# Optimization experiments

Measured on AMD Instinct MI355X. Metric: run time of the kernel, lower is better.

## Reference

```python
import jax, jax.numpy as jnp
import numpy as np

WS = 8        # window_size
SHIFT = 4     # shift_size
HEADS = 3
DIM = 96
EPS = 1e-5

# static relative coordinates for one window (matches torch.meshgrid default 'ij')
_coords = np.stack(np.meshgrid(np.arange(WS), np.arange(WS), indexing='ij'))  # [2,ws,ws]
_flat = _coords.reshape(2, -1)                                               # [2,N]
_rel = _flat[:, :, None] - _flat[:, None, :]                                  # [2,N,N]
REL_ABS_SUM = jnp.asarray(np.abs(_rel[0]) + np.abs(_rel[1]), dtype=np.float32)  # [N,N]


def _layernorm(x, g, b):
    m = jnp.mean(x, axis=-1, keepdims=True)
    v = jnp.mean((x - m) ** 2, axis=-1, keepdims=True)
    return (x - m) * jax.lax.rsqrt(v + EPS) * g + b


def _band_shift(x, s):
    # x: [B,C,H,W]. Each band of WS rows: even band index -> roll +s along W, odd -> roll -s.
    B, C, H, W = x.shape
    xb = x.reshape(B, C, H // WS, WS, W)
    ev = jnp.roll(xb, s, axis=-1)
    od = jnp.roll(xb, -s, axis=-1)
    parity = (jnp.arange(H // WS) % 2 == 1).reshape(1, 1, -1, 1, 1)
    return jnp.where(parity, od, ev).reshape(B, C, H, W)


def _window_partition(x):
    # [B,C,H,W] -> [B*nH*nW, WS*WS, C]
    B, C, H, W = x.shape
    x = x.reshape(B, C, H // WS, WS, W // WS, WS)
    x = x.transpose(0, 2, 4, 3, 5, 1)
    return x.reshape(-1, WS * WS, C)


def _window_reverse(w, B, H, W, C):
    # [B*nH*nW, WS*WS, C] -> [B,C,H,W]
    x = w.reshape(B, H // WS, W // WS, WS, WS, C)
    x = x.transpose(0, 5, 1, 3, 2, 4)
    return x.reshape(B, C, H, W)


def setup_inputs() -> dict:
    key = jax.random.key(0)
    ks = jax.random.split(key, 8)
    d = DIM
    return {
        'x': jax.random.normal(ks[0], (2, d, 512, 512), jnp.float32),
        'ln1_g': jnp.ones((d,), jnp.float32),
        'ln1_b': jnp.zeros((d,), jnp.float32),
        'qkv_w': jax.random.normal(ks[1], (3 * d, d), jnp.float32) * 0.02,
        'qkv_b': jnp.zeros((3 * d,), jnp.float32),
        'lap_A': jnp.float32(1.0),
        'lap_B': jnp.float32(1.0),
        'proj_w': jax.random.normal(ks[2], (d, d), jnp.float32) * 0.02,
        'proj_b': jnp.zeros((d,), jnp.float32),
        'ln2_g': jnp.ones((d,), jnp.float32),
        'ln2_b': jnp.zeros((d,), jnp.float32),
        'mlp_w1': jax.random.normal(ks[3], (4 * d, d), jnp.float32) * 0.02,
        'mlp_b1': jnp.zeros((4 * d,), jnp.float32),
        'mlp_w2': jax.random.normal(ks[4], (d, 4 * d), jnp.float32) * 0.02,
        'mlp_b2': jnp.zeros((d,), jnp.float32),
    }


def reference(x, ln1_g, ln1_b, qkv_w, qkv_b, lap_A, lap_B, proj_w, proj_b,
              ln2_g, ln2_b, mlp_w1, mlp_b1, mlp_w2, mlp_b2):
    B, C, H, W = x.shape
    hd = C // HEADS
    scale = hd ** -0.5

    tokens = x.transpose(0, 2, 3, 1).reshape(B, H * W, C)  # [B,HW,C]
    shortcut = tokens
    xn = _layernorm(tokens, ln1_g, ln1_b)
    xn = xn.reshape(B, H, W, C).transpose(0, 3, 1, 2)       # [B,C,H,W]

    xs = _band_shift(xn, SHIFT)
    win = _window_partition(xs)                             # [Bw, N, C]

    # window attention
    Bw, N, _ = win.shape
    qkv = win @ qkv_w.T + qkv_b                             # [Bw,N,3C]
    qkv = qkv.reshape(Bw, N, 3, HEADS, hd)
    q = qkv[:, :, 0].transpose(0, 2, 1, 3) * scale          # [Bw,h,N,hd]
    k = qkv[:, :, 1].transpose(0, 2, 1, 3)
    v = qkv[:, :, 2].transpose(0, 2, 1, 3)
    attn = jnp.einsum('bhnd,bhmd->bhnm', q, k)              # [Bw,h,N,N]
    bias = (lap_A ** 2) * jnp.exp(-0.5 * (REL_ABS_SUM / (lap_B ** 2)))  # [N,N]
    attn = jax.nn.softmax(attn + bias[None, None], axis=-1)
    out = jnp.einsum('bhnm,bhmd->bhnd', attn, v)            # [Bw,h,N,hd]
    out = out.transpose(0, 2, 1, 3).reshape(Bw, N, C)
    out = out @ proj_w.T + proj_b

    xr = _window_reverse(out, B, H, W, C)                   # [B,C,H,W]
    xr = _band_shift(xr, -SHIFT)                            # inverse shift

    xt = xr.transpose(0, 2, 3, 1).reshape(B, H * W, C)
    xt = shortcut + xt
    h1 = _layernorm(xt, ln2_g, ln2_b)
    h1 = jax.nn.gelu(h1 @ mlp_w1.T + mlp_b1, approximate=False)
    xt = xt + (h1 @ mlp_w2.T + mlp_b2)

    return xt.reshape(B, H, W, C).transpose(0, 3, 1, 2)
```

## Files before the change

kernel.cpp:

```cpp
#include <hip/hip_runtime.h>

#define SHIFT 4

typedef short bf16x8 __attribute__((ext_vector_type(8)));
typedef float f32x4  __attribute__((ext_vector_type(4)));

#define MFMA(a, b, c) __builtin_amdgcn_mfma_f32_16x16x32_bf16((a), (b), (c), 0, 0, 0)

__device__ __forceinline__ unsigned short f2bf(float f) {
  unsigned int u = __float_as_uint(f);
  u += 0x7fffu + ((u >> 16) & 1u);
  return (unsigned short)(u >> 16);
}
__device__ __forceinline__ float bf2f(unsigned short u) {
  return __uint_as_float(((unsigned int)u) << 16);
}

__global__ void k_cvt(const float* __restrict__ s, unsigned short* __restrict__ d, int n) {
  int i = blockIdx.x * blockDim.x + threadIdx.x;
  int st = gridDim.x * blockDim.x;
  for (; i < n; i += st) d[i] = f2bf(s[i]);
}

__global__ void k_cvt_p1(const float* __restrict__ s, unsigned short* __restrict__ d) {
  int i = blockIdx.x * 256 + threadIdx.x;
  if (i < 36864) {
    int col = i / 96, k = i - col * 96;
    d[(((col >> 4) * 3 + (k >> 5)) << 9) + ((col & 15) << 5) + (k & 31)] = f2bf(s[i]);
  }
}
__global__ void k_cvt_p2(const float* __restrict__ s, unsigned short* __restrict__ d) {
  int i = blockIdx.x * 256 + threadIdx.x;
  if (i < 36864) {
    int col = i / 384, k = i - col * 384;
    d[(((col >> 4) * 12 + (k >> 5)) << 9) + ((col & 15) << 5) + (k & 31)] = f2bf(s[i]);
  }
}

__global__ __launch_bounds__(256, 8) void k_pre(
    const float* __restrict__ x, unsigned short* __restrict__ X)
{
  __shared__ __align__(16) unsigned short xls[64 * 104];
  const int tid = threadIdx.x;
  const int bid = blockIdx.x;
  const int b  = bid >> 12;
  const int h  = (bid >> 3) & 511;
  const int w0 = (bid & 7) << 6;

#pragma unroll
  for (int v = 0; v < 6; ++v) {
    int idx4 = v * 256 + tid;
    int c    = idx4 >> 4;
    int p4   = (idx4 & 15) << 2;
    const float4 f = *reinterpret_cast<const float4*>(
        &x[((size_t)(b * 96 + c) << 18) + (h << 9) + w0 + p4]);
    xls[(p4 + 0) * 104 + c] = f2bf(f.x);
    xls[(p4 + 1) * 104 + c] = f2bf(f.y);
    xls[(p4 + 2) * 104 + c] = f2bf(f.z);
    xls[(p4 + 3) * 104 + c] = f2bf(f.w);
  }
  __syncthreads();
  const int q = tid & 3, t = tid >> 2;
  unsigned short* Xo = &X[(size_t)((b << 18) + (h << 9) + w0 + t) * 96 + q * 24];
#pragma unroll
  for (int v = 0; v < 3; ++v)
    *reinterpret_cast<bf16x8*>(&Xo[v * 8]) =
        *reinterpret_cast<const bf16x8*>(&xls[t * 104 + q * 24 + v * 8]);
}

__global__ __launch_bounds__(256, 4) void k_attn(
    const float* __restrict__ ln1g, const float* __restrict__ ln1b,
    const unsigned short* __restrict__ qkvw,
    const float* __restrict__ qkvb,
    const float* __restrict__ lapA, const float* __restrict__ lapB,
    const unsigned short* __restrict__ projw,
    const float* __restrict__ projb,
    unsigned short* __restrict__ X)
{
  __shared__ __align__(16) unsigned short R1[64 * 104];
  __shared__ __align__(16) unsigned short Ks[64 * 104];
  __shared__ __align__(16) unsigned short Vt[96 * 72];

  const int tid = threadIdx.x;
  const int wid = blockIdx.x;
  const int b   = wid >> 12;
  const int hi  = (wid >> 6) & 63;
  const int wi  = wid & 63;
  const int q   = tid & 3;
  const int t   = tid >> 2;
  const int lane = tid & 63;
  const int wv   = tid >> 6;
  const int l16  = lane & 15;
  const int lg   = lane >> 4;
  const int arow = wv * 16 + l16;
  const f32x4 zz = {0.f, 0.f, 0.f, 0.f};

  const int sh = ((hi & 1) == 0) ? -SHIFT : SHIFT;

  const int ftok = wv * 16 + l16;
  const int fhh = hi * 8 + (ftok >> 3);
  const int fww = ((wi * 8 + (ftok & 7)) + sh) & 511;
  const unsigned short* xfp = &X[(size_t)((b << 18) + (fhh << 9) + fww) * 96 + lg * 8];

  float xv[24];
#pragma unroll
  for (int ks = 0; ks < 3; ++ks) {
    bf16x8 g = *reinterpret_cast<const bf16x8*>(&xfp[ks * 32]);
#pragma unroll
    for (int e = 0; e < 8; ++e) xv[ks * 8 + e] = bf2f((unsigned short)g[e]);
  }
  float mu, rs;
  {
    float s1 = 0.f, s2 = 0.f;
#pragma unroll
    for (int k = 0; k < 24; ++k) { float v = xv[k]; s1 += v; s2 += v * v; }
    s1 += __shfl_xor(s1, 16); s2 += __shfl_xor(s2, 16);
    s1 += __shfl_xor(s1, 32); s2 += __shfl_xor(s2, 32);
    mu = s1 * (1.f / 96.f);
    rs = rsqrtf(s2 * (1.f / 96.f) - mu * mu + 1e-5f);
  }
  bf16x8 afr[3];
#pragma unroll
  for (int ks = 0; ks < 3; ++ks) {
#pragma unroll
    for (int e = 0; e < 8; ++e) {
      int c = ks * 32 + lg * 8 + e;
      afr[ks][e] = (short)f2bf((xv[ks * 8 + e] - mu) * rs * ln1g[c] + ln1b[c]);
    }
  }

  const float qscale = 0.17677669529663687f;
#pragma unroll
  for (int nt = 0; nt < 6; ++nt) {
    int col = nt * 16 + l16;
    f32x4 acc = zz;
#pragma unroll
    for (int ks = 0; ks < 3; ++ks)
      acc = MFMA(afr[ks], *reinterpret_cast<const bf16x8*>(&qkvw[col * 96 + ks * 32 + lg * 8]), acc);
    float bc = qkvb[col];
#pragma unroll
    for (int j = 0; j < 4; ++j)
      R1[(wv * 16 + lg * 4 + j) * 104 + col] = f2bf((acc[j] + bc) * qscale);
  }
#pragma unroll
  for (int nt = 0; nt < 6; ++nt) {
    int col = 96 + nt * 16 + l16;
    f32x4 acc = zz;
#pragma unroll
    for (int ks = 0; ks < 3; ++ks)
      acc = MFMA(afr[ks], *reinterpret_cast<const bf16x8*>(&qkvw[col * 96 + ks * 32 + lg * 8]), acc);
    float bc = qkvb[col];
#pragma unroll
    for (int j = 0; j < 4; ++j)
      Ks[(wv * 16 + lg * 4 + j) * 104 + nt * 16 + l16] = f2bf(acc[j] + bc);
  }
#pragma unroll
  for (int nt = 0; nt < 6; ++nt) {
    int col = 192 + nt * 16 + l16;
    f32x4 acc = zz;
#pragma unroll
    for (int ks = 0; ks < 3; ++ks)
      acc = MFMA(afr[ks], *reinterpret_cast<const bf16x8*>(&qkvw[col * 96 + ks * 32 + lg * 8]), acc);
    float bc = qkvb[col];
#pragma unroll
    for (int j = 0; j < 4; ++j)
      Vt[(nt * 16 + l16) * 72 + wv * 16 + lg * 4 + j] = f2bf(acc[j] + bc);
  }
  __syncthreads();

  float bias_r[4][4];
  {
    const float a = lapA[0], bb = lapB[0];
    const float A2 = a * a;
    const float nh = -0.5f / (bb * bb);
#pragma unroll
    for (int j = 0; j < 4; ++j) {
      int qi = wv * 16 + lg * 4 + j;
      int qr = qi >> 3, qc = qi & 7;
#pragma unroll
      for (int kt = 0; kt < 4; ++kt) {
        int key = kt * 16 + l16;
        int dd = abs(qr - (key >> 3)) + abs(qc - (key & 7));
        bias_r[j][kt] = A2 * __expf(nh * (float)dd);
      }
    }
  }

  bf16x8 aqh[3];
#pragma unroll
  for (int h = 0; h < 3; ++h)
    aqh[h] = *reinterpret_cast<const bf16x8*>(&R1[arow * 104 + h * 32 + lg * 8]);

  f32x4 oacc[6];
#pragma unroll
  for (int i = 0; i < 6; ++i) oacc[i] = zz;

#pragma unroll 1
  for (int h = 0; h < 3; ++h) {
    f32x4 sc[4];
#pragma unroll
    for (int kt = 0; kt < 4; ++kt) {
      bf16x8 bk = *reinterpret_cast<const bf16x8*>(&Ks[(kt * 16 + l16) * 104 + h * 32 + lg * 8]);
      sc[kt] = MFMA(aqh[h], bk, zz);
    }
#pragma unroll
    for (int j = 0; j < 4; ++j) {
      int qi = wv * 16 + lg * 4 + j;
      float e0 = __expf(sc[0][j] + bias_r[j][0]);
      float e1 = __expf(sc[1][j] + bias_r[j][1]);
      float e2 = __expf(sc[2][j] + bias_r[j][2]);
      float e3 = __expf(sc[3][j] + bias_r[j][3]);
      float s = e0 + e1 + e2 + e3;
#pragma unroll
      for (int off = 1; off < 16; off <<= 1) s += __shfl_xor(s, off);
      float inv = 1.0f / s;
      R1[qi * 104 +  0 + l16] = f2bf(e0 * inv);
      R1[qi * 104 + 16 + l16] = f2bf(e1 * inv);
      R1[qi * 104 + 32 + l16] = f2bf(e2 * inv);
      R1[qi * 104 + 48 + l16] = f2bf(e3 * inv);
    }
    bf16x8 ap0 = *reinterpret_cast<const bf16x8*>(&R1[arow * 104 +  0 + lg * 8]);
    bf16x8 ap1 = *reinterpret_cast<const bf16x8*>(&R1[arow * 104 + 32 + lg * 8]);
#pragma unroll
    for (int dt = 0; dt < 2; ++dt) {
      int vcol = h * 32 + dt * 16 + l16;
      bf16x8 bv0 = *reinterpret_cast<const bf16x8*>(&Vt[vcol * 72 +  0 + lg * 8]);
      bf16x8 bv1 = *reinterpret_cast<const bf16x8*>(&Vt[vcol * 72 + 32 + lg * 8]);
      oacc[h * 2 + dt] = MFMA(ap0, bv0, oacc[h * 2 + dt]);
      oacc[h * 2 + dt] = MFMA(ap1, bv1, oacc[h * 2 + dt]);
    }
  }
#pragma unroll
  for (int i = 0; i < 6; ++i)
#pragma unroll
    for (int j = 0; j < 4; ++j)
      R1[(wv * 16 + lg * 4 + j) * 104 + i * 16 + l16] = f2bf(oacc[i][j]);

  bf16x8 ao[3];
#pragma unroll
  for (int ks = 0; ks < 3; ++ks)
    ao[ks] = *reinterpret_cast<const bf16x8*>(&R1[arow * 104 + ks * 32 + lg * 8]);
#pragma unroll
  for (int nt = 0; nt < 6; ++nt) {
    int col = nt * 16 + l16;
    f32x4 acc = zz;
#pragma unroll
    for (int ks = 0; ks < 3; ++ks)
      acc = MFMA(ao[ks], *reinterpret_cast<const bf16x8*>(&projw[col * 96 + ks * 32 + lg * 8]), acc);
    float pb = projb[col];
#pragma unroll
    for (int j = 0; j < 4; ++j)
      R1[(wv * 16 + lg * 4 + j) * 104 + col] = f2bf(acc[j] + pb);
  }
  {
    const int hh2 = hi * 8 + (t >> 3);
    const int ww2 = ((wi * 8 + (t & 7)) + sh) & 511;
    unsigned short* xg = &X[(size_t)((b << 18) + (hh2 << 9) + ww2) * 96 + q * 24];
#pragma unroll
    for (int v = 0; v < 3; ++v) {
      bf16x8 m  = *reinterpret_cast<const bf16x8*>(&R1[t * 104 + q * 24 + v * 8]);
      bf16x8 xr = *reinterpret_cast<const bf16x8*>(&xg[v * 8]);
      bf16x8 pk;
#pragma unroll
      for (int e = 0; e < 8; ++e)
        pk[e] = (short)f2bf(bf2f((unsigned short)m[e]) + bf2f((unsigned short)xr[e]));
      *reinterpret_cast<bf16x8*>(&xg[v * 8]) = pk;
    }
  }
}

__global__ __launch_bounds__(512, 2) void k_mlp(
    const unsigned short* __restrict__ X,
    const float* __restrict__ ln2g, const float* __restrict__ ln2b,
    const unsigned short* __restrict__ w1p,
    const float* __restrict__ b1,
    const unsigned short* __restrict__ w2p,
    const float* __restrict__ b2,
    float* __restrict__ out)
{
  __shared__ __align__(16) unsigned short Wl[36864];
  __shared__ __align__(16) unsigned short W2l[34816];
  __shared__ __align__(16) unsigned short Hl[128 * 72];

  const int tid = threadIdx.x;
  const int q    = tid & 3;
  const int t    = tid >> 2;
  const int lane = tid & 63;
  const int wv   = tid >> 6;
  const int l16  = lane & 15;
  const int lg   = lane >> 4;
  const f32x4 zz = {0.f, 0.f, 0.f, 0.f};

#pragma unroll
  for (int it = 0; it < 9; ++it) {
    int v8 = it * 512 + tid;
    *reinterpret_cast<bf16x8*>(&Wl[v8 * 8]) = *reinterpret_cast<const bf16x8*>(&w1p[v8 * 8]);
    if (v8 < 4352)
      *reinterpret_cast<bf16x8*>(&W2l[v8 * 8]) = *reinterpret_cast<const bf16x8*>(&w2p[v8 * 8]);
  }
  bf16x8 wfr[4];
#pragma unroll
  for (int r = 0; r < 4; ++r)
    wfr[r] = *reinterpret_cast<const bf16x8*>(&w2p[((68 + r) << 9) + (l16 << 5) + lg * 8]);

  float gr[24], br[24], b1r[24], b2r[6];
#pragma unroll
  for (int i = 0; i < 24; ++i) {
    int c = (i >> 3) * 32 + lg * 8 + (i & 7);
    gr[i] = ln2g[c]; br[i] = ln2b[c];
  }
#pragma unroll
  for (int i = 0; i < 24; ++i) b1r[i] = b1[i * 16 + l16];
#pragma unroll
  for (int i = 0; i < 6; ++i) b2r[i] = b2[i * 16 + l16];

  __syncthreads();

#pragma unroll 1
  for (int s = 0; s < 8; ++s) {
    const int stb = (blockIdx.x * 8 + s) * 128;

    const unsigned short* xfp = &X[(size_t)(stb + wv * 16 + l16) * 96 + lg * 8];
    float xv[24];
#pragma unroll
    for (int ks = 0; ks < 3; ++ks) {
      bf16x8 g = *reinterpret_cast<const bf16x8*>(&xfp[ks * 32]);
#pragma unroll
      for (int e = 0; e < 8; ++e) xv[ks * 8 + e] = bf2f((unsigned short)g[e]);
    }
    float mu, rs;
    {
      float s1 = 0.f, s2 = 0.f;
#pragma unroll
      for (int k = 0; k < 24; ++k) { float v = xv[k]; s1 += v; s2 += v * v; }
      s1 += __shfl_xor(s1, 16); s2 += __shfl_xor(s2, 16);
      s1 += __shfl_xor(s1, 32); s2 += __shfl_xor(s2, 32);
      mu = s1 * (1.f / 96.f);
      rs = rsqrtf(s2 * (1.f / 96.f) - mu * mu + 1e-5f);
    }
    bf16x8 a1[3];
#pragma unroll
    for (int ks = 0; ks < 3; ++ks)
#pragma unroll
      for (int e = 0; e < 8; ++e)
        a1[ks][e] = (short)f2bf((xv[ks * 8 + e] - mu) * rs * gr[ks * 8 + e] + br[ks * 8 + e]);

    f32x4 acc2[6];
#pragma unroll
    for (int i = 0; i < 6; ++i) acc2[i] = zz;

#pragma unroll
    for (int ch = 0; ch < 6; ++ch) {
#pragma unroll
      for (int nt = 0; nt < 4; ++nt) {
        const int ntg = ch * 4 + nt;
        f32x4 acc = zz;
#pragma unroll
        for (int ks = 0; ks < 3; ++ks)
          acc = MFMA(a1[ks],
                     *reinterpret_cast<const bf16x8*>(&Wl[((ntg * 3 + ks) << 9) + (l16 << 5) + lg * 8]),
                     acc);
        float bb = b1r[ntg];
#pragma unroll
        for (int j = 0; j < 4; ++j) {
          float v = acc[j] + bb;
          float tt = v * fmaf(0.071354816f, v * v, 1.5957691f);
          float g = v * __builtin_amdgcn_rcpf(1.f + __expf(-tt));
          Hl[(wv * 16 + lg * 4 + j) * 72 + nt * 16 + l16] = f2bf(g);
        }
      }
      bf16x8 ah0 = *reinterpret_cast<const bf16x8*>(&Hl[(wv * 16 + l16) * 72 + lg * 8]);
      bf16x8 ah1 = *reinterpret_cast<const bf16x8*>(&Hl[(wv * 16 + l16) * 72 + 32 + lg * 8]);
#pragma unroll
      for (int nt = 0; nt < 6; ++nt) {
        const int t0 = nt * 12 + ch * 2;
        const int t1 = t0 + 1;
        bf16x8 bf0 = (t0 >= 68) ? wfr[(t0 - 68) & 3]
                   : *reinterpret_cast<const bf16x8*>(&W2l[(t0 << 9) + (l16 << 5) + lg * 8]);
        bf16x8 bf1 = (t1 >= 68) ? wfr[(t1 - 68) & 3]
                   : *reinterpret_cast<const bf16x8*>(&W2l[(t1 << 9) + (l16 << 5) + lg * 8]);
        acc2[nt] = MFMA(ah0, bf0, acc2[nt]);
        acc2[nt] = MFMA(ah1, bf1, acc2[nt]);
      }
    }

    const int tok = stb + t;
    const unsigned short* xrp = &X[(size_t)tok * 96 + q * 24];
    const int bb_ = tok >> 18;
    const int pix = tok & 262143;
#pragma unroll
    for (int pass = 0; pass < 2; ++pass) {
#pragma unroll
      for (int ntl = 0; ntl < 3; ++ntl) {
        const int nt = pass * 3 + ntl;
#pragma unroll
        for (int j = 0; j < 4; ++j)
          Hl[(wv * 16 + lg * 4 + j) * 72 + ntl * 16 + l16] = f2bf(acc2[nt][j] + b2r[nt]);
      }
      if ((q >> 1) == pass) {
        const int lc = (q & 1) * 24;
#pragma unroll
        for (int v = 0; v < 3; ++v) {
          bf16x8 m  = *reinterpret_cast<const bf16x8*>(&Hl[t * 72 + lc + v * 8]);
          bf16x8 xr = *reinterpret_cast<const bf16x8*>(&xrp[v * 8]);
#pragma unroll
          for (int e = 0; e < 8; ++e) {
            int c = q * 24 + v * 8 + e;
            out[((size_t)(bb_ * 96 + c) << 18) + pix] =
                bf2f((unsigned short)m[e]) + bf2f((unsigned short)xr[e]);
          }
        }
      }
    }
  }
}

extern "C" void kernel_launch(void* const* d_in, const int* in_sizes, int n_in,
                              void* d_out, int out_size, void* d_ws, size_t ws_size,
                              hipStream_t stream) {
  const float* x     = (const float*)d_in[0];
  const float* ln1g  = (const float*)d_in[1];
  const float* ln1b  = (const float*)d_in[2];
  const float* qkv_w = (const float*)d_in[3];
  const float* qkv_b = (const float*)d_in[4];
  const float* lapA  = (const float*)d_in[5];
  const float* lapB  = (const float*)d_in[6];
  const float* prj_w = (const float*)d_in[7];
  const float* prj_b = (const float*)d_in[8];
  const float* ln2g  = (const float*)d_in[9];
  const float* ln2b  = (const float*)d_in[10];
  const float* w1f   = (const float*)d_in[11];
  const float* b1    = (const float*)d_in[12];
  const float* w2f   = (const float*)d_in[13];
  const float* b2    = (const float*)d_in[14];

  char* ws = (char*)d_ws;
  unsigned short* X     = (unsigned short*)ws;
  unsigned short* qkvwb = (unsigned short*)(ws + 100663296);
  unsigned short* prjwb = (unsigned short*)(ws + 100718592);
  unsigned short* w1p   = (unsigned short*)(ws + 100737024);
  unsigned short* w2p   = (unsigned short*)(ws + 100810752);

  k_cvt   <<<64, 256, 0, stream>>>(qkv_w, qkvwb, 288 * 96);
  k_cvt   <<<64, 256, 0, stream>>>(prj_w, prjwb, 96 * 96);
  k_cvt_p1<<<144, 256, 0, stream>>>(w1f, w1p);
  k_cvt_p2<<<144, 256, 0, stream>>>(w2f, w2p);

  k_pre <<<8192, 256, 0, stream>>>(x, X);
  k_attn<<<8192, 256, 0, stream>>>(ln1g, ln1b, qkvwb, qkv_b, lapA, lapB,
                                   prjwb, prj_b, X);
  k_mlp <<<512, 512, 0, stream>>>(X, ln2g, ln2b, w1p, b1, w2p, b2,
                                  (float*)d_out);
}
```

Measured before the change: 512.6 us.

## Batch weight loads, reuse register residual, move barrier after bias compute

The QKV and projection GEMMs now load weight fragments in batches of nine before issuing MFMAs, so global load latency overlaps instead of serialising per tile. The residual add reuses the x values already held in registers from the LayerNorm load and writes back through the same per-lane pointer, which removes a second global read of X. The barrier moves after the bias computation, and f2bf now uses the HIP intrinsic conversion. Holding nine weight fragments raises register pressure, and each lane now writes R1 rows it did not produce itself, which relies on the barriers that already exist.

```diff
diff --git a/kernel.cpp b/kernel.cpp
--- a/kernel.cpp
+++ b/kernel.cpp
@@ -1,4 +1,5 @@
 #include <hip/hip_runtime.h>
+#include <hip/hip_bf16.h>
 
 #define SHIFT 4
 
@@ -8,9 +9,8 @@
 #define MFMA(a, b, c) __builtin_amdgcn_mfma_f32_16x16x32_bf16((a), (b), (c), 0, 0, 0)
 
 __device__ __forceinline__ unsigned short f2bf(float f) {
-  unsigned int u = __float_as_uint(f);
-  u += 0x7fffu + ((u >> 16) & 1u);
-  return (unsigned short)(u >> 16);
+  __hip_bfloat16 h = __float2bfloat16(f);
+  return __hip_bfloat16_raw(h).x;
 }
 __device__ __forceinline__ float bf2f(unsigned short u) {
   return __uint_as_float(((unsigned int)u) << 16);
@@ -86,8 +86,6 @@
   const int b   = wid >> 12;
   const int hi  = (wid >> 6) & 63;
   const int wi  = wid & 63;
-  const int q   = tid & 3;
-  const int t   = tid >> 2;
   const int lane = tid & 63;
   const int wv   = tid >> 6;
   const int l16  = lane & 15;
@@ -100,7 +98,7 @@
   const int ftok = wv * 16 + l16;
   const int fhh = hi * 8 + (ftok >> 3);
   const int fww = ((wi * 8 + (ftok & 7)) + sh) & 511;
-  const unsigned short* xfp = &X[(size_t)((b << 18) + (fhh << 9) + fww) * 96 + lg * 8];
+  unsigned short* xfp = &X[(size_t)((b << 18) + (fhh << 9) + fww) * 96 + lg * 8];
 
   float xv[24];
 #pragma unroll
@@ -131,42 +129,67 @@
 
   const float qscale = 0.17677669529663687f;
 #pragma unroll
-  for (int nt = 0; nt < 6; ++nt) {
-    int col = nt * 16 + l16;
-    f32x4 acc = zz;
-#pragma unroll
-    for (int ks = 0; ks < 3; ++ks)
-      acc = MFMA(afr[ks], *reinterpret_cast<const bf16x8*>(&qkvw[col * 96 + ks * 32 + lg * 8]), acc);
-    float bc = qkvb[col];
-#pragma unroll
-    for (int j = 0; j < 4; ++j)
-      R1[(wv * 16 + lg * 4 + j) * 104 + col] = f2bf((acc[j] + bc) * qscale);
-  }
-#pragma unroll
-  for (int nt = 0; nt < 6; ++nt) {
-    int col = 96 + nt * 16 + l16;
-    f32x4 acc = zz;
-#pragma unroll
-    for (int ks = 0; ks < 3; ++ks)
-      acc = MFMA(afr[ks], *reinterpret_cast<const bf16x8*>(&qkvw[col * 96 + ks * 32 + lg * 8]), acc);
-    float bc = qkvb[col];
-#pragma unroll
-    for (int j = 0; j < 4; ++j)
-      Ks[(wv * 16 + lg * 4 + j) * 104 + nt * 16 + l16] = f2bf(acc[j] + bc);
-  }
-#pragma unroll
-  for (int nt = 0; nt < 6; ++nt) {
-    int col = 192 + nt * 16 + l16;
-    f32x4 acc = zz;
-#pragma unroll
-    for (int ks = 0; ks < 3; ++ks)
-      acc = MFMA(afr[ks], *reinterpret_cast<const bf16x8*>(&qkvw[col * 96 + ks * 32 + lg * 8]), acc);
-    float bc = qkvb[col];
-#pragma unroll
-    for (int j = 0; j < 4; ++j)
-      Vt[(nt * 16 + l16) * 72 + wv * 16 + lg * 4 + j] = f2bf(acc[j] + bc);
-  }
-  __syncthreads();
+  for (int half = 0; half < 2; ++half) {
+    bf16x8 wf[9];
+#pragma unroll
+    for (int i = 0; i < 9; ++i) {
+      int col = (half * 3 + i / 3) * 16 + l16;
+      wf[i] = *reinterpret_cast<const bf16x8*>(&qkvw[col * 96 + (i % 3) * 32 + lg * 8]);
+    }
+#pragma unroll
+    for (int ntl = 0; ntl < 3; ++ntl) {
+      int col = (half * 3 + ntl) * 16 + l16;
+      f32x4 acc = zz;
+#pragma unroll
+      for (int ks = 0; ks < 3; ++ks) acc = MFMA(afr[ks], wf[ntl * 3 + ks], acc);
+      float bc = qkvb[col];
+#pragma unroll
+      for (int j = 0; j < 4; ++j)
+        R1[(wv * 16 + lg * 4 + j) * 104 + col] = f2bf((acc[j] + bc) * qscale);
+    }
+  }
+#pragma unroll
+  for (int half = 0; half < 2; ++half) {
+    bf16x8 wf[9];
+#pragma unroll
+    for (int i = 0; i < 9; ++i) {
+      int col = 96 + (half * 3 + i / 3) * 16 + l16;
+      wf[i] = *reinterpret_cast<const bf16x8*>(&qkvw[col * 96 + (i % 3) * 32 + lg * 8]);
+    }
+#pragma unroll
+    for (int ntl = 0; ntl < 3; ++ntl) {
+      int nt = half * 3 + ntl;
+      int col = 96 + nt * 16 + l16;
+      f32x4 acc = zz;
+#pragma unroll
+      for (int ks = 0; ks < 3; ++ks) acc = MFMA(afr[ks], wf[ntl * 3 + ks], acc);
+      float bc = qkvb[col];
+#pragma unroll
+      for (int j = 0; j < 4; ++j)
+        Ks[(wv * 16 + lg * 4 + j) * 104 + nt * 16 + l16] = f2bf(acc[j] + bc);
+    }
+  }
+#pragma unroll
+  for (int half = 0; half < 2; ++half) {
+    bf16x8 wf[9];
+#pragma unroll
+    for (int i = 0; i < 9; ++i) {
+      int col = 192 + (half * 3 + i / 3) * 16 + l16;
+      wf[i] = *reinterpret_cast<const bf16x8*>(&qkvw[col * 96 + (i % 3) * 32 + lg * 8]);
+    }
+#pragma unroll
+    for (int ntl = 0; ntl < 3; ++ntl) {
+      int nt = half * 3 + ntl;
+      int col = 192 + nt * 16 + l16;
+      f32x4 acc = zz;
+#pragma unroll
+      for (int ks = 0; ks < 3; ++ks) acc = MFMA(afr[ks], wf[ntl * 3 + ks], acc);
+      float bc = qkvb[col];
+#pragma unroll
+      for (int j = 0; j < 4; ++j)
+        Vt[(nt * 16 + l16) * 72 + wv * 16 + lg * 4 + j] = f2bf(acc[j] + bc);
+    }
+  }
 
   float bias_r[4][4];
   {
@@ -185,6 +208,7 @@
       }
     }
   }
+  __syncthreads();
 
   bf16x8 aqh[3];
 #pragma unroll
@@ -241,31 +265,33 @@
   for (int ks = 0; ks < 3; ++ks)
     ao[ks] = *reinterpret_cast<const bf16x8*>(&R1[arow * 104 + ks * 32 + lg * 8]);
 #pragma unroll
-  for (int nt = 0; nt < 6; ++nt) {
-    int col = nt * 16 + l16;
-    f32x4 acc = zz;
-#pragma unroll
-    for (int ks = 0; ks < 3; ++ks)
-      acc = MFMA(ao[ks], *reinterpret_cast<const bf16x8*>(&projw[col * 96 + ks * 32 + lg * 8]), acc);
-    float pb = projb[col];
-#pragma unroll
-    for (int j = 0; j < 4; ++j)
-      R1[(wv * 16 + lg * 4 + j) * 104 + col] = f2bf(acc[j] + pb);
-  }
-  {
-    const int hh2 = hi * 8 + (t >> 3);
-    const int ww2 = ((wi * 8 + (t & 7)) + sh) & 511;
-    unsigned short* xg = &X[(size_t)((b << 18) + (hh2 << 9) + ww2) * 96 + q * 24];
-#pragma unroll
-    for (int v = 0; v < 3; ++v) {
-      bf16x8 m  = *reinterpret_cast<const bf16x8*>(&R1[t * 104 + q * 24 + v * 8]);
-      bf16x8 xr = *reinterpret_cast<const bf16x8*>(&xg[v * 8]);
-      bf16x8 pk;
-#pragma unroll
-      for (int e = 0; e < 8; ++e)
-        pk[e] = (short)f2bf(bf2f((unsigned short)m[e]) + bf2f((unsigned short)xr[e]));
-      *reinterpret_cast<bf16x8*>(&xg[v * 8]) = pk;
-    }
+  for (int half = 0; half < 2; ++half) {
+    bf16x8 wf[9];
+#pragma unroll
+    for (int i = 0; i < 9; ++i) {
+      int col = (half * 3 + i / 3) * 16 + l16;
+      wf[i] = *reinterpret_cast<const bf16x8*>(&projw[col * 96 + (i % 3) * 32 + lg * 8]);
+    }
+#pragma unroll
+    for (int ntl = 0; ntl < 3; ++ntl) {
+      int col = (half * 3 + ntl) * 16 + l16;
+      f32x4 acc = zz;
+#pragma unroll
+      for (int ks = 0; ks < 3; ++ks) acc = MFMA(ao[ks], wf[ntl * 3 + ks], acc);
+      float pb = projb[col];
+#pragma unroll
+      for (int j = 0; j < 4; ++j)
+        R1[(wv * 16 + lg * 4 + j) * 104 + col] = f2bf(acc[j] + pb);
+    }
+  }
+#pragma unroll
+  for (int ks = 0; ks < 3; ++ks) {
+    bf16x8 m = *reinterpret_cast<const bf16x8*>(&R1[ftok * 104 + ks * 32 + lg * 8]);
+    bf16x8 pk;
+#pragma unroll
+    for (int e = 0; e < 8; ++e)
+      pk[e] = (short)f2bf(bf2f((unsigned short)m[e]) + xv[ks * 8 + e]);
+    *reinterpret_cast<bf16x8*>(&xfp[ks * 32]) = pk;
   }
 }
 
```

Result: no change. 513.4 us (+0.2%).

## Make attention kernel persistent with LDS-resident packed weights and prefetch

Applied to the files above, without the earlier changes.

The attention kernel becomes persistent: 256 blocks of 512 threads, each holding two window groups that loop over 16 windows. The QKV and projection weights are repacked into an MFMA-friendly tiled layout and loaded into LDS once per block instead of being read from global memory per window. LayerNorm parameters and biases are hoisted into registers, and the next window's input is prefetched during attention. The residual now reuses the input values already held in registers instead of re-reading X. The cost is one block per CU with heavy LDS use, extra barriers, and possibly lower latency hiding.

```diff
diff --git a/kernel.cpp b/kernel.cpp
--- a/kernel.cpp
+++ b/kernel.cpp
@@ -1,4 +1,5 @@
 #include <hip/hip_runtime.h>
+#include <hip/hip_bf16.h>
 
 #define SHIFT 4
 
@@ -8,23 +9,16 @@
 #define MFMA(a, b, c) __builtin_amdgcn_mfma_f32_16x16x32_bf16((a), (b), (c), 0, 0, 0)
 
 __device__ __forceinline__ unsigned short f2bf(float f) {
-  unsigned int u = __float_as_uint(f);
-  u += 0x7fffu + ((u >> 16) & 1u);
-  return (unsigned short)(u >> 16);
+  __hip_bfloat16 h = __float2bfloat16(f);
+  return __hip_bfloat16_raw(h).x;
 }
 __device__ __forceinline__ float bf2f(unsigned short u) {
   return __uint_as_float(((unsigned int)u) << 16);
 }
 
-__global__ void k_cvt(const float* __restrict__ s, unsigned short* __restrict__ d, int n) {
-  int i = blockIdx.x * blockDim.x + threadIdx.x;
-  int st = gridDim.x * blockDim.x;
-  for (; i < n; i += st) d[i] = f2bf(s[i]);
-}
-
-__global__ void k_cvt_p1(const float* __restrict__ s, unsigned short* __restrict__ d) {
+__global__ void k_cvt_pt(const float* __restrict__ s, unsigned short* __restrict__ d, int n) {
   int i = blockIdx.x * 256 + threadIdx.x;
-  if (i < 36864) {
+  if (i < n) {
     int col = i / 96, k = i - col * 96;
     d[(((col >> 4) * 3 + (k >> 5)) << 9) + ((col & 15) << 5) + (k & 31)] = f2bf(s[i]);
   }
@@ -68,105 +62,62 @@
         *reinterpret_cast<const bf16x8*>(&xls[t * 104 + q * 24 + v * 8]);
 }
 
-__global__ __launch_bounds__(256, 4) void k_attn(
+__global__ __launch_bounds__(512, 1) void k_attn(
     const float* __restrict__ ln1g, const float* __restrict__ ln1b,
-    const unsigned short* __restrict__ qkvw,
+    const unsigned short* __restrict__ qkvwp,
     const float* __restrict__ qkvb,
     const float* __restrict__ lapA, const float* __restrict__ lapB,
-    const unsigned short* __restrict__ projw,
+    const unsigned short* __restrict__ projwp,
     const float* __restrict__ projb,
     unsigned short* __restrict__ X)
 {
-  __shared__ __align__(16) unsigned short R1[64 * 104];
-  __shared__ __align__(16) unsigned short Ks[64 * 104];
-  __shared__ __align__(16) unsigned short Vt[96 * 72];
-
-  const int tid = threadIdx.x;
-  const int wid = blockIdx.x;
-  const int b   = wid >> 12;
-  const int hi  = (wid >> 6) & 63;
-  const int wi  = wid & 63;
-  const int q   = tid & 3;
-  const int t   = tid >> 2;
+  __shared__ __align__(16) unsigned short WqkvL[27648];
+  __shared__ __align__(16) unsigned short WprojL[9216];
+  __shared__ __align__(16) unsigned short R1s[2][6656];
+  __shared__ __align__(16) unsigned short Kss[2][6656];
+  __shared__ __align__(16) unsigned short Vts[2][6912];
+
+  const int tid  = threadIdx.x;
   const int lane = tid & 63;
-  const int wv   = tid >> 6;
+  const int wv8  = tid >> 6;
+  const int g    = wv8 >> 2;
+  const int wvg  = wv8 & 3;
   const int l16  = lane & 15;
   const int lg   = lane >> 4;
-  const int arow = wv * 16 + l16;
+  const int arow = wvg * 16 + l16;
   const f32x4 zz = {0.f, 0.f, 0.f, 0.f};
 
-  const int sh = ((hi & 1) == 0) ? -SHIFT : SHIFT;
-
-  const int ftok = wv * 16 + l16;
-  const int fhh = hi * 8 + (ftok >> 3);
-  const int fww = ((wi * 8 + (ftok & 7)) + sh) & 511;
-  const unsigned short* xfp = &X[(size_t)((b << 18) + (fhh << 9) + fww) * 96 + lg * 8];
-
-  float xv[24];
-#pragma unroll
-  for (int ks = 0; ks < 3; ++ks) {
-    bf16x8 g = *reinterpret_cast<const bf16x8*>(&xfp[ks * 32]);
-#pragma unroll
-    for (int e = 0; e < 8; ++e) xv[ks * 8 + e] = bf2f((unsigned short)g[e]);
-  }
-  float mu, rs;
-  {
-    float s1 = 0.f, s2 = 0.f;
-#pragma unroll
-    for (int k = 0; k < 24; ++k) { float v = xv[k]; s1 += v; s2 += v * v; }
-    s1 += __shfl_xor(s1, 16); s2 += __shfl_xor(s2, 16);
-    s1 += __shfl_xor(s1, 32); s2 += __shfl_xor(s2, 32);
-    mu = s1 * (1.f / 96.f);
-    rs = rsqrtf(s2 * (1.f / 96.f) - mu * mu + 1e-5f);
-  }
-  bf16x8 afr[3];
-#pragma unroll
-  for (int ks = 0; ks < 3; ++ks) {
-#pragma unroll
-    for (int e = 0; e < 8; ++e) {
-      int c = ks * 32 + lg * 8 + e;
-      afr[ks][e] = (short)f2bf((xv[ks * 8 + e] - mu) * rs * ln1g[c] + ln1b[c]);
-    }
-  }
-
-  const float qscale = 0.17677669529663687f;
-#pragma unroll
-  for (int nt = 0; nt < 6; ++nt) {
-    int col = nt * 16 + l16;
-    f32x4 acc = zz;
-#pragma unroll
-    for (int ks = 0; ks < 3; ++ks)
-      acc = MFMA(afr[ks], *reinterpret_cast<const bf16x8*>(&qkvw[col * 96 + ks * 32 + lg * 8]), acc);
-    float bc = qkvb[col];
-#pragma unroll
-    for (int j = 0; j < 4; ++j)
-      R1[(wv * 16 + lg * 4 + j) * 104 + col] = f2bf((acc[j] + bc) * qscale);
-  }
-#pragma unroll
-  for (int nt = 0; nt < 6; ++nt) {
-    int col = 96 + nt * 16 + l16;
-    f32x4 acc = zz;
-#pragma unroll
-    for (int ks = 0; ks < 3; ++ks)
-      acc = MFMA(afr[ks], *reinterpret_cast<const bf16x8*>(&qkvw[col * 96 + ks * 32 + lg * 8]), acc);
-    float bc = qkvb[col];
-#pragma unroll
-    for (int j = 0; j < 4; ++j)
-      Ks[(wv * 16 + lg * 4 + j) * 104 + nt * 16 + l16] = f2bf(acc[j] + bc);
-  }
-#pragma unroll
-  for (int nt = 0; nt < 6; ++nt) {
-    int col = 192 + nt * 16 + l16;
-    f32x4 acc = zz;
-#pragma unroll
-    for (int ks = 0; ks < 3; ++ks)
-      acc = MFMA(afr[ks], *reinterpret_cast<const bf16x8*>(&qkvw[col * 96 + ks * 32 + lg * 8]), acc);
-    float bc = qkvb[col];
-#pragma unroll
-    for (int j = 0; j < 4; ++j)
-      Vt[(nt * 16 + l16) * 72 + wv * 16 + lg * 4 + j] = f2bf(acc[j] + bc);
-  }
-  __syncthreads();
+  unsigned short* R1 = R1s[g];
+  unsigned short* Ks = Kss[g];
+  unsigned short* Vt = Vts[g];
+
+#pragma unroll
+  for (int it = 0; it < 7; ++it) {
+    int v8 = it * 512 + tid;
+    if (v8 < 3456)
+      *reinterpret_cast<bf16x8*>(&WqkvL[v8 * 8]) =
+          *reinterpret_cast<const bf16x8*>(&qkvwp[v8 * 8]);
+  }
+#pragma unroll
+  for (int it = 0; it < 3; ++it) {
+    int v8 = it * 512 + tid;
+    if (v8 < 1152)
+      *reinterpret_cast<bf16x8*>(&WprojL[v8 * 8]) =
+          *reinterpret_cast<const bf16x8*>(&projwp[v8 * 8]);
+  }
+
+  float gl[24], bl[24];
+#pragma unroll
+  for (int i = 0; i < 24; ++i) {
+    int c = (i >> 3) * 32 + lg * 8 + (i & 7);
+    gl[i] = ln1g[c]; bl[i] = ln1b[c];
+  }
+  float qb[18];
+#pragma unroll
+  for (int nt = 0; nt < 18; ++nt) qb[nt] = qkvb[nt * 16 + l16];
+  float pbr[6];
+#pragma unroll
+  for (int nt = 0; nt < 6; ++nt) pbr[nt] = projb[nt * 16 + l16];
 
   float bias_r[4][4];
   {
@@ -175,7 +126,7 @@
     const float nh = -0.5f / (bb * bb);
 #pragma unroll
     for (int j = 0; j < 4; ++j) {
-      int qi = wv * 16 + lg * 4 + j;
+      int qi = wvg * 16 + lg * 4 + j;
       int qr = qi >> 3, qc = qi & 7;
 #pragma unroll
       for (int kt = 0; kt < 4; ++kt) {
@@ -185,87 +136,165 @@
       }
     }
   }
-
-  bf16x8 aqh[3];
-#pragma unroll
-  for (int h = 0; h < 3; ++h)
-    aqh[h] = *reinterpret_cast<const bf16x8*>(&R1[arow * 104 + h * 32 + lg * 8]);
-
-  f32x4 oacc[6];
-#pragma unroll
-  for (int i = 0; i < 6; ++i) oacc[i] = zz;
+  __syncthreads();
+
+  const float qscale = 0.17677669529663687f;
+  const int ftok = wvg * 16 + l16;
+
+  auto xaddr = [&](int w) -> unsigned short* {
+    int b  = w >> 12;
+    int hi = (w >> 6) & 63;
+    int wi = w & 63;
+    int sh = ((hi & 1) == 0) ? -SHIFT : SHIFT;
+    int fhh = hi * 8 + (ftok >> 3);
+    int fww = ((wi * 8 + (ftok & 7)) + sh) & 511;
+    return &X[(size_t)((b << 18) + (fhh << 9) + fww) * 96 + lg * 8];
+  };
+
+  int w = blockIdx.x * 32 + g;
+  unsigned short* xfp = xaddr(w);
+  bf16x8 xn[3];
+#pragma unroll
+  for (int ks = 0; ks < 3; ++ks)
+    xn[ks] = *reinterpret_cast<const bf16x8*>(&xfp[ks * 32]);
 
 #pragma unroll 1
-  for (int h = 0; h < 3; ++h) {
-    f32x4 sc[4];
-#pragma unroll
-    for (int kt = 0; kt < 4; ++kt) {
-      bf16x8 bk = *reinterpret_cast<const bf16x8*>(&Ks[(kt * 16 + l16) * 104 + h * 32 + lg * 8]);
-      sc[kt] = MFMA(aqh[h], bk, zz);
-    }
-#pragma unroll
-    for (int j = 0; j < 4; ++j) {
-      int qi = wv * 16 + lg * 4 + j;
-      float e0 = __expf(sc[0][j] + bias_r[j][0]);
-      float e1 = __expf(sc[1][j] + bias_r[j][1]);
-      float e2 = __expf(sc[2][j] + bias_r[j][2]);
-      float e3 = __expf(sc[3][j] + bias_r[j][3]);
-      float s = e0 + e1 + e2 + e3;
-#pragma unroll
-      for (int off = 1; off < 16; off <<= 1) s += __shfl_xor(s, off);
-      float inv = 1.0f / s;
-      R1[qi * 104 +  0 + l16] = f2bf(e0 * inv);
-      R1[qi * 104 + 16 + l16] = f2bf(e1 * inv);
-      R1[qi * 104 + 32 + l16] = f2bf(e2 * inv);
-      R1[qi * 104 + 48 + l16] = f2bf(e3 * inv);
-    }
-    bf16x8 ap0 = *reinterpret_cast<const bf16x8*>(&R1[arow * 104 +  0 + lg * 8]);
-    bf16x8 ap1 = *reinterpret_cast<const bf16x8*>(&R1[arow * 104 + 32 + lg * 8]);
-#pragma unroll
-    for (int dt = 0; dt < 2; ++dt) {
-      int vcol = h * 32 + dt * 16 + l16;
-      bf16x8 bv0 = *reinterpret_cast<const bf16x8*>(&Vt[vcol * 72 +  0 + lg * 8]);
-      bf16x8 bv1 = *reinterpret_cast<const bf16x8*>(&Vt[vcol * 72 + 32 + lg * 8]);
-      oacc[h * 2 + dt] = MFMA(ap0, bv0, oacc[h * 2 + dt]);
-      oacc[h * 2 + dt] = MFMA(ap1, bv1, oacc[h * 2 + dt]);
-    }
-  }
-#pragma unroll
-  for (int i = 0; i < 6; ++i)
-#pragma unroll
-    for (int j = 0; j < 4; ++j)
-      R1[(wv * 16 + lg * 4 + j) * 104 + i * 16 + l16] = f2bf(oacc[i][j]);
-
-  bf16x8 ao[3];
-#pragma unroll
-  for (int ks = 0; ks < 3; ++ks)
-    ao[ks] = *reinterpret_cast<const bf16x8*>(&R1[arow * 104 + ks * 32 + lg * 8]);
-#pragma unroll
-  for (int nt = 0; nt < 6; ++nt) {
-    int col = nt * 16 + l16;
-    f32x4 acc = zz;
+  for (int it = 0; it < 16; ++it) {
+    float xv[24];
 #pragma unroll
     for (int ks = 0; ks < 3; ++ks)
-      acc = MFMA(ao[ks], *reinterpret_cast<const bf16x8*>(&projw[col * 96 + ks * 32 + lg * 8]), acc);
-    float pb = projb[col];
-#pragma unroll
-    for (int j = 0; j < 4; ++j)
-      R1[(wv * 16 + lg * 4 + j) * 104 + col] = f2bf(acc[j] + pb);
-  }
-  {
-    const int hh2 = hi * 8 + (t >> 3);
-    const int ww2 = ((wi * 8 + (t & 7)) + sh) & 511;
-    unsigned short* xg = &X[(size_t)((b << 18) + (hh2 << 9) + ww2) * 96 + q * 24];
-#pragma unroll
-    for (int v = 0; v < 3; ++v) {
-      bf16x8 m  = *reinterpret_cast<const bf16x8*>(&R1[t * 104 + q * 24 + v * 8]);
-      bf16x8 xr = *reinterpret_cast<const bf16x8*>(&xg[v * 8]);
+#pragma unroll
+      for (int e = 0; e < 8; ++e) xv[ks * 8 + e] = bf2f((unsigned short)xn[ks][e]);
+
+    float mu, rs;
+    {
+      float s1 = 0.f, s2 = 0.f;
+#pragma unroll
+      for (int k = 0; k < 24; ++k) { float v = xv[k]; s1 += v; s2 += v * v; }
+      s1 += __shfl_xor(s1, 16); s2 += __shfl_xor(s2, 16);
+      s1 += __shfl_xor(s1, 32); s2 += __shfl_xor(s2, 32);
+      mu = s1 * (1.f / 96.f);
+      rs = rsqrtf(s2 * (1.f / 96.f) - mu * mu + 1e-5f);
+    }
+    bf16x8 afr[3];
+#pragma unroll
+    for (int ks = 0; ks < 3; ++ks)
+#pragma unroll
+      for (int e = 0; e < 8; ++e)
+        afr[ks][e] = (short)f2bf((xv[ks * 8 + e] - mu) * rs * gl[ks * 8 + e] + bl[ks * 8 + e]);
+
+#pragma unroll
+    for (int nt = 0; nt < 18; ++nt) {
+      f32x4 acc = zz;
+#pragma unroll
+      for (int ks = 0; ks < 3; ++ks)
+        acc = MFMA(afr[ks],
+                   *reinterpret_cast<const bf16x8*>(&WqkvL[((nt * 3 + ks) << 9) + (l16 << 5) + lg * 8]),
+                   acc);
+      float bc = qb[nt];
+      if (nt < 6) {
+#pragma unroll
+        for (int j = 0; j < 4; ++j)
+          R1[(wvg * 16 + lg * 4 + j) * 104 + nt * 16 + l16] = f2bf((acc[j] + bc) * qscale);
+      } else if (nt < 12) {
+#pragma unroll
+        for (int j = 0; j < 4; ++j)
+          Ks[(wvg * 16 + lg * 4 + j) * 104 + (nt - 6) * 16 + l16] = f2bf(acc[j] + bc);
+      } else {
+#pragma unroll
+        for (int j = 0; j < 4; ++j)
+          Vt[((nt - 12) * 16 + l16) * 72 + wvg * 16 + lg * 4 + j] = f2bf(acc[j] + bc);
+      }
+    }
+    __syncthreads();
+
+    int wn = w + 2;
+    if (wn > 8191) wn = w;
+    unsigned short* xfpn = xaddr(wn);
+#pragma unroll
+    for (int ks = 0; ks < 3; ++ks)
+      xn[ks] = *reinterpret_cast<const bf16x8*>(&xfpn[ks * 32]);
+
+    bf16x8 aqh[3];
+#pragma unroll
+    for (int h = 0; h < 3; ++h)
+      aqh[h] = *reinterpret_cast<const bf16x8*>(&R1[arow * 104 + h * 32 + lg * 8]);
+
+    f32x4 oacc[6];
+#pragma unroll
+    for (int i = 0; i < 6; ++i) oacc[i] = zz;
+
+#pragma unroll 1
+    for (int h = 0; h < 3; ++h) {
+      f32x4 sc[4];
+#pragma unroll
+      for (int kt = 0; kt < 4; ++kt) {
+        bf16x8 bk = *reinterpret_cast<const bf16x8*>(&Ks[(kt * 16 + l16) * 104 + h * 32 + lg * 8]);
+        sc[kt] = MFMA(aqh[h], bk, zz);
+      }
+#pragma unroll
+      for (int j = 0; j < 4; ++j) {
+        int qi = wvg * 16 + lg * 4 + j;
+        float e0 = __expf(sc[0][j] + bias_r[j][0]);
+        float e1 = __expf(sc[1][j] + bias_r[j][1]);
+        float e2 = __expf(sc[2][j] + bias_r[j][2]);
+        float e3 = __expf(sc[3][j] + bias_r[j][3]);
+        float s = e0 + e1 + e2 + e3;
+#pragma unroll
+        for (int off = 1; off < 16; off <<= 1) s += __shfl_xor(s, off);
+        float inv = 1.0f / s;
+        R1[qi * 104 +  0 + l16] = f2bf(e0 * inv);
+        R1[qi * 104 + 16 + l16] = f2bf(e1 * inv);
+        R1[qi * 104 + 32 + l16] = f2bf(e2 * inv);
+        R1[qi * 104 + 48 + l16] = f2bf(e3 * inv);
+      }
+      bf16x8 ap0 = *reinterpret_cast<const bf16x8*>(&R1[arow * 104 +  0 + lg * 8]);
+      bf16x8 ap1 = *reinterpret_cast<const bf16x8*>(&R1[arow * 104 + 32 + lg * 8]);
+#pragma unroll
+      for (int dt = 0; dt < 2; ++dt) {
+        int vcol = h * 32 + dt * 16 + l16;
+        bf16x8 bv0 = *reinterpret_cast<const bf16x8*>(&Vt[vcol * 72 +  0 + lg * 8]);
+        bf16x8 bv1 = *reinterpret_cast<const bf16x8*>(&Vt[vcol * 72 + 32 + lg * 8]);
+        oacc[h * 2 + dt] = MFMA(ap0, bv0, oacc[h * 2 + dt]);
+        oacc[h * 2 + dt] = MFMA(ap1, bv1, oacc[h * 2 + dt]);
+      }
+    }
+    __syncthreads();
+
+#pragma unroll
+    for (int i = 0; i < 6; ++i)
+#pragma unroll
+      for (int j = 0; j < 4; ++j)
+        R1[(wvg * 16 + lg * 4 + j) * 104 + i * 16 + l16] = f2bf(oacc[i][j]);
+
+    bf16x8 ao[3];
+#pragma unroll
+    for (int ks = 0; ks < 3; ++ks)
+      ao[ks] = *reinterpret_cast<const bf16x8*>(&R1[arow * 104 + ks * 32 + lg * 8]);
+#pragma unroll
+    for (int nt = 0; nt < 6; ++nt) {
+      f32x4 acc = zz;
+#pragma unroll
+      for (int ks = 0; ks < 3; ++ks)
+        acc = MFMA(ao[ks],
+                   *reinterpret_cast<const bf16x8*>(&WprojL[((nt * 3 + ks) << 9) + (l16 << 5) + lg * 8]),
+                   acc);
+      float pb = pbr[nt];
+#pragma unroll
+      for (int j = 0; j < 4; ++j)
+        R1[(wvg * 16 + lg * 4 + j) * 104 + nt * 16 + l16] = f2bf(acc[j] + pb);
+    }
+#pragma unroll
+    for (int ks = 0; ks < 3; ++ks) {
+      bf16x8 m = *reinterpret_cast<const bf16x8*>(&R1[ftok * 104 + ks * 32 + lg * 8]);
       bf16x8 pk;
 #pragma unroll
       for (int e = 0; e < 8; ++e)
-        pk[e] = (short)f2bf(bf2f((unsigned short)m[e]) + bf2f((unsigned short)xr[e]));
-      *reinterpret_cast<bf16x8*>(&xg[v * 8]) = pk;
-    }
+        pk[e] = (short)f2bf(bf2f((unsigned short)m[e]) + xv[ks * 8 + e]);
+      *reinterpret_cast<bf16x8*>(&xfp[ks * 32]) = pk;
+    }
+    xfp = xfpn;
+    w = wn;
   }
 }
 
@@ -324,9 +353,9 @@
     float xv[24];
 #pragma unroll
     for (int ks = 0; ks < 3; ++ks) {
-      bf16x8 g = *reinterpret_cast<const bf16x8*>(&xfp[ks * 32]);
-#pragma unroll
-      for (int e = 0; e < 8; ++e) xv[ks * 8 + e] = bf2f((unsigned short)g[e]);
+      bf16x8 g2 = *reinterpret_cast<const bf16x8*>(&xfp[ks * 32]);
+#pragma unroll
+      for (int e = 0; e < 8; ++e) xv[ks * 8 + e] = bf2f((unsigned short)g2[e]);
     }
     float mu, rs;
     {
@@ -365,8 +394,8 @@
         for (int j = 0; j < 4; ++j) {
           float v = acc[j] + bb;
           float tt = v * fmaf(0.071354816f, v * v, 1.5957691f);
-          float g = v * __builtin_amdgcn_rcpf(1.f + __expf(-tt));
-          Hl[(wv * 16 + lg * 4 + j) * 72 + nt * 16 + l16] = f2bf(g);
+          float gg = v * __builtin_amdgcn_rcpf(1.f + __expf(-tt));
+          Hl[(wv * 16 + lg * 4 + j) * 72 + nt * 16 + l16] = f2bf(gg);
         }
       }
       bf16x8 ah0 = *reinterpret_cast<const bf16x8*>(&Hl[(wv * 16 + l16) * 72 + lg * 8]);
@@ -436,19 +465,19 @@
 
   char* ws = (char*)d_ws;
   unsigned short* X     = (unsigned short*)ws;
-  unsigned short* qkvwb = (unsigned short*)(ws + 100663296);
-  unsigned short* prjwb = (unsigned short*)(ws + 100718592);
+  unsigned short* qkvwp = (unsigned short*)(ws + 100663296);
+  unsigned short* prjwp = (unsigned short*)(ws + 100718592);
   unsigned short* w1p   = (unsigned short*)(ws + 100737024);
   unsigned short* w2p   = (unsigned short*)(ws + 100810752);
 
-  k_cvt   <<<64, 256, 0, stream>>>(qkv_w, qkvwb, 288 * 96);
-  k_cvt   <<<64, 256, 0, stream>>>(prj_w, prjwb, 96 * 96);
-  k_cvt_p1<<<144, 256, 0, stream>>>(w1f, w1p);
+  k_cvt_pt<<<108, 256, 0, stream>>>(qkv_w, qkvwp, 288 * 96);
+  k_cvt_pt<<<36,  256, 0, stream>>>(prj_w, prjwp, 96 * 96);
+  k_cvt_pt<<<144, 256, 0, stream>>>(w1f,   w1p,   384 * 96);
   k_cvt_p2<<<144, 256, 0, stream>>>(w2f, w2p);
 
   k_pre <<<8192, 256, 0, stream>>>(x, X);
-  k_attn<<<8192, 256, 0, stream>>>(ln1g, ln1b, qkvwb, qkv_b, lapA, lapB,
-                                   prjwb, prj_b, X);
+  k_attn<<<256, 512, 0, stream>>>(ln1g, ln1b, qkvwp, qkv_b, lapA, lapB,
+                                  prjwp, prj_b, X);
   k_mlp <<<512, 512, 0, stream>>>(X, ln2g, ln2b, w1p, b1, w2p, b2,
                                   (float*)d_out);
 }
```

New measurement: 467.4 us. 8.8% less time.
